# Optimization experiments

Measured on AMD Instinct MI355X. Metric: run time of the kernel, lower is better.

## Reference

```python
import jax, jax.numpy as jnp
import numpy as np

B, N, C, MAX_L = 8, 4096, 16, 3  # batch, num_atoms, num_channels, max SO(3) degree


def setup_inputs() -> dict:
    key = jax.random.key(0)
    ks = jax.random.split(key, 2 * (MAX_L + 1))
    inp = {}
    for l in range(MAX_L + 1):
        inp[f"p{l}_re"] = jax.random.normal(ks[2 * l], (B, N, 2 * l + 1, C), dtype=jnp.float32)
        inp[f"p{l}_im"] = jax.random.normal(ks[2 * l + 1], (B, N, 2 * l + 1, C), dtype=jnp.float32)
    return inp


def _forward(parts):
    # parts: list of (re, im) pairs, each (B, N, 2l+1, C)
    re0, im0 = parts[0]
    b, n, _, c = re0.shape
    # torch.view_as_real(parts[0]).reshape(b, n, 2C): channels interleaved as re0,im0,re1,im1,...
    part0 = jnp.stack([re0[:, :, 0, :], im0[:, :, 0, :]], axis=-1).reshape(b, n, 2 * c)
    norms = []
    for re, im in parts:
        # Gram over the m (2l+1) dim: G[c1,c2] = sum_m v[:,m,c1] * conj(v[:,m,c2])
        g_re = jnp.einsum('bnmc,bnmd->bncd', re, re) + jnp.einsum('bnmc,bnmd->bncd', im, im)
        g_im = jnp.einsum('bnmc,bnmd->bncd', im, re) - jnp.einsum('bnmc,bnmd->bncd', re, im)
        # channel flattening matches torch loop order: index = channel1*C + channel2
        norms.append((g_re + 1j * g_im).astype(jnp.complex64).reshape(b, n, c * c))
    return jnp.concatenate([part0.astype(jnp.complex64)] + norms, axis=-1)


def reference(p0_re, p0_im, p1_re, p1_im, p2_re, p2_im, p3_re, p3_im):
    parts = [(p0_re, p0_im), (p1_re, p1_im), (p2_re, p2_im), (p3_re, p3_im)]
    return _forward(parts)
```

## Files before the change

kernel.cpp:

```cpp
#include <hip/hip_runtime.h>


typedef float fx4 __attribute__((ext_vector_type(4)));

#define PADW 520

__global__ __launch_bounds__(256) void getscalars_real_v7(
    const float* __restrict__ p0re, const float* __restrict__ p0im,
    const float* __restrict__ p1re, const float* __restrict__ p1im,
    const float* __restrict__ p2re, const float* __restrict__ p2im,
    const float* __restrict__ p3re, const float* __restrict__ p3im,
    float* __restrict__ out)
{
    const int t = threadIdx.x;
    const size_t a0 = (size_t)blockIdx.x * 4;

    __shared__ float s[4 * PADW];

    #pragma unroll
    for (int k2 = 0; k2 < 2; ++k2) {
        const int id = t + k2 * 256;
        const int al = id >> 7;
        const int tt = id & 127;
        const size_t a = a0 + al;
        const fx4* src; int off;
        if (tt < 8)       { src = (const fx4*)((tt < 4   ? p0re : p0im) + a * 16);  off = tt & 3; }
        else if (tt < 32) { src = (const fx4*)((tt < 20  ? p1re : p1im) + a * 48);  off = (tt < 20)  ? tt - 8  : tt - 20; }
        else if (tt < 72) { src = (const fx4*)((tt < 52  ? p2re : p2im) + a * 80);  off = (tt < 52)  ? tt - 32 : tt - 52; }
        else              { src = (const fx4*)((tt < 100 ? p3re : p3im) + a * 112); off = (tt < 100) ? tt - 72 : tt - 100; }
        ((fx4*)(s + al * PADW))[tt] = src[off];
    }
    __syncthreads();

    fx4* oq = (fx4*)out;

    if (t < 32) {
        const int al = t >> 3;
        const int j  = t & 7;
        const float* sa = s + al * PADW;
        fx4 v = { sa[2 * j], sa[16 + 2 * j], sa[2 * j + 1], sa[16 + 2 * j + 1] };
        oq[(a0 + al) * 264 + j] = v;
    }

    const int e   = t & 63;
    const int w   = t >> 6;
    const int k   = e >> 4;
    const int li  = e & 15;
    const int tr4 = (li >> 2) << 2;
    const int tcq = li & 3;
    const float* sa = s + k * PADW;
    const size_t abase = (a0 + k) * 264 + 8 + (size_t)w * 64;

#define GS_TILE(RO, IO, M)                                                    \
    {                                                                         \
        fx4 acc0 = {0,0,0,0}, acc1 = {0,0,0,0};                               \
        fx4 acc2 = {0,0,0,0}, acc3 = {0,0,0,0};                               \
        _Pragma("unroll")                                                     \
        for (int m = 0; m < (M); ++m) {                                       \
            const fx4 r1 = *(const fx4*)(sa + (RO) + m * 16 + tr4);           \
            const fx4 i1 = *(const fx4*)(sa + (IO) + m * 16 + tr4);           \
            const fx4 r2 = *(const fx4*)(sa + (RO) + m * 16 + tcq * 4);       \
            const fx4 i2 = *(const fx4*)(sa + (IO) + m * 16 + tcq * 4);       \
            acc0 += r1.x * r2 + i1.x * i2;                                    \
            acc1 += r1.y * r2 + i1.y * i2;                                    \
            acc2 += r1.z * r2 + i1.z * i2;                                    \
            acc3 += r1.w * r2 + i1.w * i2;                                    \
        }                                                                     \
        oq[abase + (tr4 + 0) * 4 + tcq] = acc0;                               \
        oq[abase + (tr4 + 1) * 4 + tcq] = acc1;                               \
        oq[abase + (tr4 + 2) * 4 + tcq] = acc2;                               \
        oq[abase + (tr4 + 3) * 4 + tcq] = acc3;                               \
    }

    if      (w == 0) GS_TILE(0,   16,  1)
    else if (w == 1) GS_TILE(32,  80,  3)
    else if (w == 2) GS_TILE(128, 208, 5)
    else             GS_TILE(288, 400, 7)
#undef GS_TILE
}


__global__ __launch_bounds__(256) void getscalars_real_v2(
    const float* __restrict__ p0re, const float* __restrict__ p0im,
    const float* __restrict__ p1re, const float* __restrict__ p1im,
    const float* __restrict__ p2re, const float* __restrict__ p2im,
    const float* __restrict__ p3re, const float* __restrict__ p3im,
    float* __restrict__ out, int abase)
{
    const int t = threadIdx.x;
    const size_t a = (size_t)blockIdx.x + abase;

    __shared__ float s[512];
    fx4* s4 = (fx4*)s;

    if (t < 128) {
        const fx4* src; int off;
        if (t < 8)       { src = (const fx4*)((t < 4   ? p0re : p0im) + a * 16);  off = t & 3; }
        else if (t < 32) { src = (const fx4*)((t < 20  ? p1re : p1im) + a * 48);  off = (t < 20)  ? t - 8  : t - 20; }
        else if (t < 72) { src = (const fx4*)((t < 52  ? p2re : p2im) + a * 80);  off = (t < 52)  ? t - 32 : t - 52; }
        else             { src = (const fx4*)((t < 100 ? p3re : p3im) + a * 112); off = (t < 100) ? t - 72 : t - 100; }
        s4[t] = src[off];
    }
    __syncthreads();

    fx4* obase = (fx4*)(out + a * 1056);

    if (t < 8) {
        fx4 v = { s[2 * t], s[16 + 2 * t], s[2 * t + 1], s[16 + 2 * t + 1] };
        obase[t] = v;
    }

    const int e  = t & 63;
    const int c1 = e >> 2;
    const int q2 = e & 3;
    const int w  = t >> 6;

    fx4 acc = { 0.0f, 0.0f, 0.0f, 0.0f };

#define GS_GRAM_Q(RO, IO, M)                                                  \
    {                                                                         \
        _Pragma("unroll")                                                     \
        for (int m = 0; m < (M); ++m) {                                       \
            const float r1 = s[(RO) + m * 16 + c1];                           \
            const float i1 = s[(IO) + m * 16 + c1];                           \
            const fx4   r2 = s4[((RO) >> 2) + m * 4 + q2];                    \
            const fx4   i2 = s4[((IO) >> 2) + m * 4 + q2];                    \
            acc += r1 * r2 + i1 * i2;                                         \
        }                                                                     \
    }

    if      (w == 0) GS_GRAM_Q(0,   16,  1)
    else if (w == 1) GS_GRAM_Q(32,  80,  3)
    else if (w == 2) GS_GRAM_Q(128, 208, 5)
    else             GS_GRAM_Q(288, 400, 7)
#undef GS_GRAM_Q

    obase[8 + w * 64 + e] = acc;
}

extern "C" void kernel_launch(void* const* d_in, const int* in_sizes, int n_in,
                              void* d_out, int out_size, void* d_ws, size_t ws_size,
                              hipStream_t stream) {
    const float* p0re = (const float*)d_in[0];
    const float* p0im = (const float*)d_in[1];
    const float* p1re = (const float*)d_in[2];
    const float* p1im = (const float*)d_in[3];
    const float* p2re = (const float*)d_in[4];
    const float* p2im = (const float*)d_in[5];
    const float* p3re = (const float*)d_in[6];
    const float* p3im = (const float*)d_in[7];
    float* out = (float*)d_out;

    const int atoms  = in_sizes[0] / 16;
    const int blocks = atoms >> 2;
    const int tail   = atoms & 3;

    if (blocks > 0) {
        getscalars_real_v7<<<blocks, 256, 0, stream>>>(
            p0re, p0im, p1re, p1im, p2re, p2im, p3re, p3im, out);
    }
    if (tail > 0) {
        getscalars_real_v2<<<tail, 256, 0, stream>>>(
            p0re, p0im, p1re, p1im, p2re, p2im, p3re, p3im, out, blocks * 4);
    }
}
```

Before: 36.66 us.

## Convert to persistent grid-stride kernel with double-buffered LDS prefetch

Replaces the one-block-per-4-atoms kernel with a persistent kernel capped at 2048 blocks. Each block loops over atom groups and prefetches the next group's inputs into registers while it computes the current one, then writes them into the other LDS buffer. The aim is to hide global load latency and cut block launch overhead. In exchange it doubles the LDS use per block and leaves fewer blocks in flight, which may lower the memory-level parallelism this bandwidth-bound kernel depends on.

```diff
diff --git a/kernel.cpp b/kernel.cpp
--- a/kernel.cpp
+++ b/kernel.cpp
@@ -5,42 +5,51 @@
 
 #define PADW 520
 
-__global__ __launch_bounds__(256) void getscalars_real_v7(
+__device__ __forceinline__ void map_src(
+    int id,
     const float* __restrict__ p0re, const float* __restrict__ p0im,
     const float* __restrict__ p1re, const float* __restrict__ p1im,
     const float* __restrict__ p2re, const float* __restrict__ p2im,
     const float* __restrict__ p3re, const float* __restrict__ p3im,
-    float* __restrict__ out)
+    const float** pe, size_t* st, int* al_out, int* tt_out)
+{
+    const int al = id >> 7, tt = id & 127;
+    const float* arr; int S, off;
+    if (tt < 8)       { arr = (tt < 4   ? p0re : p0im); S = 16;  off = tt & 3; }
+    else if (tt < 32) { arr = (tt < 20  ? p1re : p1im); S = 48;  off = (tt < 20)  ? tt - 8  : tt - 20; }
+    else if (tt < 72) { arr = (tt < 52  ? p2re : p2im); S = 80;  off = (tt < 52)  ? tt - 32 : tt - 52; }
+    else              { arr = (tt < 100 ? p3re : p3im); S = 112; off = (tt < 100) ? tt - 72 : tt - 100; }
+    *pe = arr + (size_t)al * S + (size_t)off * 4;
+    *st = (size_t)S * 4;
+    *al_out = al; *tt_out = tt;
+}
+
+__global__ __launch_bounds__(256) void getscalars_real_v8(
+    const float* __restrict__ p0re, const float* __restrict__ p0im,
+    const float* __restrict__ p1re, const float* __restrict__ p1im,
+    const float* __restrict__ p2re, const float* __restrict__ p2im,
+    const float* __restrict__ p3re, const float* __restrict__ p3im,
+    float* __restrict__ out, int ngroups)
 {
     const int t = threadIdx.x;
-    const size_t a0 = (size_t)blockIdx.x * 4;
-
-    __shared__ float s[4 * PADW];
-
-    #pragma unroll
-    for (int k2 = 0; k2 < 2; ++k2) {
-        const int id = t + k2 * 256;
-        const int al = id >> 7;
-        const int tt = id & 127;
-        const size_t a = a0 + al;
-        const fx4* src; int off;
-        if (tt < 8)       { src = (const fx4*)((tt < 4   ? p0re : p0im) + a * 16);  off = tt & 3; }
-        else if (tt < 32) { src = (const fx4*)((tt < 20  ? p1re : p1im) + a * 48);  off = (tt < 20)  ? tt - 8  : tt - 20; }
-        else if (tt < 72) { src = (const fx4*)((tt < 52  ? p2re : p2im) + a * 80);  off = (tt < 52)  ? tt - 32 : tt - 52; }
-        else              { src = (const fx4*)((tt < 100 ? p3re : p3im) + a * 112); off = (tt < 100) ? tt - 72 : tt - 100; }
-        ((fx4*)(s + al * PADW))[tt] = src[off];
-    }
+
+    __shared__ float s[2][4 * PADW];
+
+    const float *pe0, *pe1; size_t st0, st1; int al0, tt0, al1, tt1;
+    map_src(t,       p0re, p0im, p1re, p1im, p2re, p2im, p3re, p3im,
+            &pe0, &st0, &al0, &tt0);
+    map_src(t + 256, p0re, p0im, p1re, p1im, p2re, p2im, p3re, p3im,
+            &pe1, &st1, &al1, &tt1);
+
+    const int gstep = gridDim.x;
+    int g = blockIdx.x;
+    if (g >= ngroups) return;
+
+    fx4 r0 = *(const fx4*)(pe0 + (size_t)g * st0);
+    fx4 r1 = *(const fx4*)(pe1 + (size_t)g * st1);
+    ((fx4*)(s[0] + al0 * PADW))[tt0] = r0;
+    ((fx4*)(s[0] + al1 * PADW))[tt1] = r1;
     __syncthreads();
-
-    fx4* oq = (fx4*)out;
-
-    if (t < 32) {
-        const int al = t >> 3;
-        const int j  = t & 7;
-        const float* sa = s + al * PADW;
-        fx4 v = { sa[2 * j], sa[16 + 2 * j], sa[2 * j + 1], sa[16 + 2 * j + 1] };
-        oq[(a0 + al) * 264 + j] = v;
-    }
 
     const int e   = t & 63;
     const int w   = t >> 6;
@@ -48,23 +57,24 @@
     const int li  = e & 15;
     const int tr4 = (li >> 2) << 2;
     const int tcq = li & 3;
-    const float* sa = s + k * PADW;
-    const size_t abase = (a0 + k) * 264 + 8 + (size_t)w * 64;
-
-#define GS_TILE(RO, IO, M)                                                    \
+
+    fx4* oq = (fx4*)out;
+    int buf = 0;
+
+#define GS_TILE(SA, RO, IO, M)                                                \
     {                                                                         \
         fx4 acc0 = {0,0,0,0}, acc1 = {0,0,0,0};                               \
         fx4 acc2 = {0,0,0,0}, acc3 = {0,0,0,0};                               \
         _Pragma("unroll")                                                     \
         for (int m = 0; m < (M); ++m) {                                       \
-            const fx4 r1 = *(const fx4*)(sa + (RO) + m * 16 + tr4);           \
-            const fx4 i1 = *(const fx4*)(sa + (IO) + m * 16 + tr4);           \
-            const fx4 r2 = *(const fx4*)(sa + (RO) + m * 16 + tcq * 4);       \
-            const fx4 i2 = *(const fx4*)(sa + (IO) + m * 16 + tcq * 4);       \
-            acc0 += r1.x * r2 + i1.x * i2;                                    \
-            acc1 += r1.y * r2 + i1.y * i2;                                    \
-            acc2 += r1.z * r2 + i1.z * i2;                                    \
-            acc3 += r1.w * r2 + i1.w * i2;                                    \
+            const fx4 r1v = *(const fx4*)((SA) + (RO) + m * 16 + tr4);        \
+            const fx4 i1v = *(const fx4*)((SA) + (IO) + m * 16 + tr4);        \
+            const fx4 r2v = *(const fx4*)((SA) + (RO) + m * 16 + tcq * 4);    \
+            const fx4 i2v = *(const fx4*)((SA) + (IO) + m * 16 + tcq * 4);    \
+            acc0 += r1v.x * r2v + i1v.x * i2v;                                \
+            acc1 += r1v.y * r2v + i1v.y * i2v;                                \
+            acc2 += r1v.z * r2v + i1v.z * i2v;                                \
+            acc3 += r1v.w * r2v + i1v.w * i2v;                                \
         }                                                                     \
         oq[abase + (tr4 + 0) * 4 + tcq] = acc0;                               \
         oq[abase + (tr4 + 1) * 4 + tcq] = acc1;                               \
@@ -72,10 +82,43 @@
         oq[abase + (tr4 + 3) * 4 + tcq] = acc3;                               \
     }
 
-    if      (w == 0) GS_TILE(0,   16,  1)
-    else if (w == 1) GS_TILE(32,  80,  3)
-    else if (w == 2) GS_TILE(128, 208, 5)
-    else             GS_TILE(288, 400, 7)
+    while (true) {
+        const int gn = g + gstep;
+        const bool more = (gn < ngroups);
+        if (more) {
+            r0 = *(const fx4*)(pe0 + (size_t)gn * st0);
+            r1 = *(const fx4*)(pe1 + (size_t)gn * st1);
+        }
+
+        const float* sb = s[buf];
+        const size_t a0 = (size_t)g * 4;
+
+        if (t < 32) {
+            const int al = t >> 3;
+            const int j  = t & 7;
+            const float* sa0 = sb + al * PADW;
+            fx4 v = { sa0[2 * j], sa0[16 + 2 * j],
+                      sa0[2 * j + 1], sa0[16 + 2 * j + 1] };
+            oq[(a0 + al) * 264 + j] = v;
+        }
+
+        const float* sa = sb + k * PADW;
+        const size_t abase = (a0 + k) * 264 + 8 + (size_t)w * 64;
+
+        if      (w == 0) GS_TILE(sa, 0,   16,  1)
+        else if (w == 1) GS_TILE(sa, 32,  80,  3)
+        else if (w == 2) GS_TILE(sa, 128, 208, 5)
+        else             GS_TILE(sa, 288, 400, 7)
+
+        if (more) {
+            ((fx4*)(s[buf ^ 1] + al0 * PADW))[tt0] = r0;
+            ((fx4*)(s[buf ^ 1] + al1 * PADW))[tt1] = r1;
+        }
+        __syncthreads();
+        if (!more) break;
+        buf ^= 1;
+        g = gn;
+    }
 #undef GS_TILE
 }
 
@@ -151,16 +194,17 @@
     const float* p3im = (const float*)d_in[7];
     float* out = (float*)d_out;
 
-    const int atoms  = in_sizes[0] / 16;
-    const int blocks = atoms >> 2;
-    const int tail   = atoms & 3;
-
-    if (blocks > 0) {
-        getscalars_real_v7<<<blocks, 256, 0, stream>>>(
-            p0re, p0im, p1re, p1im, p2re, p2im, p3re, p3im, out);
+    const int atoms   = in_sizes[0] / 16;
+    const int ngroups = atoms >> 2;
+    const int tail    = atoms & 3;
+
+    if (ngroups > 0) {
+        const int nblk = ngroups < 2048 ? ngroups : 2048;
+        getscalars_real_v8<<<nblk, 256, 0, stream>>>(
+            p0re, p0im, p1re, p1im, p2re, p2im, p3re, p3im, out, ngroups);
     }
     if (tail > 0) {
         getscalars_real_v2<<<tail, 256, 0, stream>>>(
-            p0re, p0im, p1re, p1im, p2re, p2im, p3re, p3im, out, blocks * 4);
-    }
-}
+            p0re, p0im, p1re, p1im, p2re, p2im, p3re, p3im, out, ngroups * 4);
+    }
+}
```

After: 36.96 us. About the same (+0.8%).
